# Kernel optimization log

Measured on AMD Instinct MI355X. Metric: run time of the kernel, lower is better.

The kernel has to match this reference:

```python
import jax, jax.numpy as jnp
import numpy as np

G = 32; N = G * G          # gridsize, num_nodes per graph
A = 16                      # n_agents
B = 32                      # batch_size
E = 4096                    # edges per graph (~4-neighbor grid)
F_IN = 16                   # input_dim
H = 64                      # hidden_dim
L = 3                       # n_graph_layers
MID = F_IN + L * H          # 208
CAT = 2 * MID + H           # 480
MIN_VAL = -1e8


def _layer_norm(x, g, b, eps=1e-5):
    m = x.mean(-1, keepdims=True)
    v = x.var(-1, keepdims=True)
    return (x - m) * jax.lax.rsqrt(v + eps) * g + b


def setup_inputs() -> dict:
    key = jax.random.key(0)
    ks = jax.random.split(key, 16)
    inp = {}
    inp["graph_nodes"] = jax.random.normal(ks[0], (B, N, F_IN), jnp.float32)
    inp["graph_edge_links"] = jax.random.randint(ks[1], (B, 2, E), 0, N)
    inp["agent_locations"] = jax.random.randint(ks[2], (B, A), 0, N)
    inp["mask"] = jax.random.bernoulli(ks[3], 0.5, (B, A * N))
    inp["dist_matrix"] = jax.random.uniform(ks[4], (N, N), jnp.float32)
    dims = [F_IN] + [H] * L
    k = 5
    for l in range(L):
        inp[f"conv{l}_W"] = jax.random.normal(ks[k], (dims[l], H), jnp.float32) * 0.05
        inp[f"conv{l}_b"] = jnp.zeros((H,), jnp.float32)
        inp[f"conv{l}_g"] = jnp.ones((H,), jnp.float32)
        inp[f"conv{l}_beta"] = jnp.zeros((H,), jnp.float32)
        k += 1
    inp["edges_W"] = jax.random.normal(ks[k], (1, H), jnp.float32) * 0.05
    inp["edges_b"] = jnp.zeros((H,), jnp.float32)
    inp["actor1_W"] = jax.random.normal(ks[k + 1], (CAT, MID), jnp.float32) * 0.05
    inp["actor1_b"] = jnp.zeros((MID,), jnp.float32)
    inp["bn_g"] = jnp.ones((MID,), jnp.float32)
    inp["bn_b"] = jnp.zeros((MID,), jnp.float32)
    inp["actor2_W"] = jax.random.normal(ks[k + 2], (MID, 1), jnp.float32) * 0.05
    inp["actor2_b"] = jnp.zeros((1,), jnp.float32)
    return inp


def reference(graph_nodes, graph_edge_links, agent_locations, mask, dist_matrix,
              conv0_W, conv0_b, conv0_g, conv0_beta,
              conv1_W, conv1_b, conv1_g, conv1_beta,
              conv2_W, conv2_b, conv2_g, conv2_beta,
              edges_W, edges_b, actor1_W, actor1_b, bn_g, bn_b,
              actor2_W, actor2_b):
    # --- batch graphs: offset node indices per graph (Batch.from_data_list) ---
    x = graph_nodes.reshape(B * N, F_IN)
    offs = (jnp.arange(B) * N)[:, None, None]
    ei = (graph_edge_links + offs).transpose(1, 0, 2).reshape(2, B * E)
    src, dst = ei[0], ei[1]

    conv_params = [(conv0_W, conv0_b, conv0_g, conv0_beta),
                   (conv1_W, conv1_b, conv1_g, conv1_beta),
                   (conv2_W, conv2_b, conv2_g, conv2_beta)]
    outs = [x]
    for W, bb, g, beta in conv_params:
        # GINConv with eps=-1: (1+eps)*x_i == 0, so out = mlp(sum_j x_j)
        agg = jax.ops.segment_sum(x[src], dst, num_segments=B * N)
        x = jax.nn.relu(_layer_norm(agg @ W + bb, g, beta))  # mlp relu; outer .relu() idempotent
        outs.append(x)
    xc = jnp.concatenate(outs, axis=1).reshape(B, N, MID)

    # --- all-pairs (agent, node) feature build ---
    a = jnp.take_along_axis(xc, agent_locations[:, :, None], axis=1)  # [B, A, MID]
    a = jnp.repeat(a, N, axis=1)                                      # [B, A*N, MID]
    bfeat = jnp.tile(xc, (1, A, 1))                                   # [B, A*N, MID]
    c = dist_matrix[agent_locations].reshape(B, A * N, 1)             # [B, A*N, 1]
    c = c @ edges_W + edges_b                                         # [B, A*N, H]
    h = jnp.concatenate([a, bfeat, c], axis=2).reshape(-1, CAT)

    h = h @ actor1_W + actor1_b
    mu = h.mean(0)
    var = h.var(0)
    h = (h - mu) * jax.lax.rsqrt(var + 1e-5) * bn_g + bn_b  # BatchNorm1d, training stats
    h = jax.nn.relu(h)
    logits = (h @ actor2_W + actor2_b).reshape(B, A * N)
    logits = jnp.where(mask, logits, MIN_VAL)
    return jax.nn.softmax(logits, axis=1)
```

## Files before the change

### kernel.cpp

```cpp
#include <hip/hip_runtime.h>
#include <cstddef>

#define B_    32
#define N_    1024
#define E_    4096
#define A_    16
#define FIN_  16
#define H_    64
#define MID_  208
#define NODES (B_ * N_)
#define NEDGE (B_ * E_)
#define ROWS  (B_ * A_ * N_)
#define AN_   (A_ * N_)

__device__ __forceinline__ float readlane_f(float v, int l) {
  return __uint_as_float(__builtin_amdgcn_readlane(__float_as_uint(v), l));
}

__global__ __launch_bounds__(256) void k_front(const int* __restrict__ el,
                                               const float* __restrict__ dist,
                                               const int* __restrict__ loc,
                                               const float* __restrict__ W1,
                                               const float* __restrict__ eW,
                                               const float* __restrict__ eb,
                                               const float* __restrict__ b1,
                                               int* __restrict__ rowptr,
                                               int* __restrict__ counts,
                                               int* __restrict__ ssrc,
                                               float* __restrict__ d1row,
                                               float* __restrict__ c2row,
                                               float* __restrict__ e1,
                                               float* __restrict__ cu,
                                               float* __restrict__ base) {
  __shared__ int cnt[1024];
  __shared__ int cur[1024];
  __shared__ int part[256];
  __shared__ int ssrcS[4096];
  __shared__ int loc_s[16];
  int blk = blockIdx.x, t = threadIdx.x;
  if (blk < 32) {
    int b = blk;
    for (int i = t; i < 1024; i += 256) cnt[i] = 0;
    __syncthreads();
    const int* srcp = el + b * (2 * E_);
    const int* dstp = srcp + E_;
    for (int i = t; i < E_; i += 256) atomicAdd(&cnt[dstp[i]], 1);
    __syncthreads();
    int4 c4 = *(const int4*)&cnt[t * 4];
    int s = c4.x + c4.y + c4.z + c4.w;
    part[t] = s;
    __syncthreads();
    for (int off = 1; off < 256; off <<= 1) {
      int v = (t >= off) ? part[t - off] : 0;
      __syncthreads();
      part[t] += v;
      __syncthreads();
    }
    int prev = (t == 0) ? 0 : part[t - 1];
    int p0 = prev, p1 = p0 + c4.x, p2 = p1 + c4.y, p3 = p2 + c4.z;
    *(int4*)&rowptr[b * 1024 + t * 4] = make_int4(p0 + b * E_, p1 + b * E_, p2 + b * E_, p3 + b * E_);
    *(int4*)&counts[b * 1024 + t * 4] = c4;
    cur[t * 4 + 0] = p0;
    cur[t * 4 + 1] = p1;
    cur[t * 4 + 2] = p2;
    cur[t * 4 + 3] = p3;
    __syncthreads();
    for (int i = t; i < E_; i += 256) {
      int dl = dstp[i];
      int sl = srcp[i];
      int pos = atomicAdd(&cur[dl], 1);
      ssrcS[pos] = b * N_ + sl;
    }
    __syncthreads();
    for (int i = t; i < E_; i += 256) ssrc[b * E_ + i] = ssrcS[i];
  } else if (blk < 288) {
    int lane = t & 63, w = t >> 6;
    int r = (blk - 32) * 4 + w;
    const float* dr = dist + (size_t)r * N_;
    float s = 0.f, c2 = 0.f;
#pragma unroll
    for (int k = 0; k < 16; k++) {
      float v = dr[lane + 64 * k];
      s += v;
      c2 = fmaf(v, v, c2);
    }
#pragma unroll
    for (int o = 32; o > 0; o >>= 1) { s += __shfl_xor(s, o); c2 += __shfl_xor(c2, o); }
    if (lane == 0) { d1row[r] = s; c2row[r] = c2; }
  } else if (blk < 320) {
    int b = blk - 288;
    if (t < 16) loc_s[t] = loc[b * 16 + t];
    __syncthreads();
    float e4[4] = {0.f, 0.f, 0.f, 0.f};
    for (int a = 0; a < 16; a++) {
      const float* dr = dist + (size_t)loc_s[a] * N_;
#pragma unroll
      for (int k = 0; k < 4; k++) e4[k] += dr[t + 256 * k];
    }
#pragma unroll
    for (int k = 0; k < 4; k++) e1[b * N_ + t + 256 * k] = e4[k];
  } else {
    int j = t;
    if (j < MID_) {
      float c = 0.f, bs = 0.f;
      for (int k = 0; k < H_; k++) {
        float w = W1[(2 * MID_ + k) * MID_ + j];
        c = fmaf(eW[k], w, c);
        bs = fmaf(eb[k], w, bs);
      }
      cu[j] = c;
      base[j] = bs + b1[j];
    }
  }
}

template <int FINT, bool COPYIN>
__global__ __launch_bounds__(256) void k_layer(const float* __restrict__ xin, int xstride, int in_off,
                                               float* __restrict__ xc, int out_off,
                                               const int* __restrict__ rowptr,
                                               const int* __restrict__ counts,
                                               const int* __restrict__ ssrc,
                                               const float* __restrict__ W,
                                               const float* __restrict__ bias,
                                               const float* __restrict__ g,
                                               const float* __restrict__ beta) {
  int t = threadIdx.x, lane = t & 63, w = t >> 6;
  float Wcol[FINT];
#pragma unroll
  for (int f = 0; f < FINT; f++) Wcol[f] = W[f * 64 + lane];
  float bv = bias[lane], gv = g[lane], bev = beta[lane];
  constexpr int CH = 64 / FINT;
  int f = lane & (FINT - 1);
  int ch = (FINT == 64) ? 0 : (lane >> 4);
  int blk = blockIdx.x;
  int xcd = blk & 7, kk = blk >> 3;
  int graph = xcd * 4 + (kk >> 5);
  int nblk = kk & 31;
  int nbase = graph * N_ + nblk * 32 + w * 8;

  float agg[8];
#pragma unroll
  for (int nn = 0; nn < 8; nn++) {
    int node = nbase + nn;
    int r0 = rowptr[node];
    int deg = counts[node];
    float a0 = 0.f, a1 = 0.f, a2 = 0.f, a3 = 0.f;
    int e = ch;
    for (; e + 3 * CH < deg; e += 4 * CH) {
      int s0 = ssrc[r0 + e];
      int s1 = ssrc[r0 + e + CH];
      int s2 = ssrc[r0 + e + 2 * CH];
      int s3 = ssrc[r0 + e + 3 * CH];
      a0 += xin[(size_t)s0 * xstride + in_off + f];
      a1 += xin[(size_t)s1 * xstride + in_off + f];
      a2 += xin[(size_t)s2 * xstride + in_off + f];
      a3 += xin[(size_t)s3 * xstride + in_off + f];
    }
    for (; e < deg; e += CH) {
      int s = ssrc[r0 + e];
      a0 += xin[(size_t)s * xstride + in_off + f];
    }
    agg[nn] = (a0 + a1) + (a2 + a3);
  }

#pragma unroll
  for (int nn = 0; nn < 8; nn++) {
    int node = nbase + nn;
    float aggf = agg[nn];
    float y0 = bv, y1 = 0.f, y2 = 0.f, y3 = 0.f;
#pragma unroll
    for (int l = 0; l < 64; l += 4) {
      y0 = fmaf(readlane_f(aggf, l + 0), Wcol[(l + 0) & (FINT - 1)], y0);
      y1 = fmaf(readlane_f(aggf, l + 1), Wcol[(l + 1) & (FINT - 1)], y1);
      y2 = fmaf(readlane_f(aggf, l + 2), Wcol[(l + 2) & (FINT - 1)], y2);
      y3 = fmaf(readlane_f(aggf, l + 3), Wcol[(l + 3) & (FINT - 1)], y3);
    }
    float y = (y0 + y1) + (y2 + y3);
    float m = y;
#pragma unroll
    for (int o = 32; o > 0; o >>= 1) m += __shfl_xor(m, o);
    m *= (1.f / 64.f);
    float d = y - m;
    float vv = d * d;
#pragma unroll
    for (int o = 32; o > 0; o >>= 1) vv += __shfl_xor(vv, o);
    vv *= (1.f / 64.f);
    float outv = fmaxf(d * rsqrtf(vv + 1e-5f) * gv + bev, 0.f);
    xc[(size_t)node * MID_ + out_off + lane] = outv;
    if (COPYIN) {
      if (lane < FIN_) xc[(size_t)node * MID_ + lane] = xin[(size_t)node * FIN_ + lane];
    }
  }
}

template <int NR>
__device__ __forceinline__ void gemm_sc(const float* __restrict__ xc,
                                        const float* __restrict__ W1,
                                        int row0w, int j0, float acc[NR][4]) {
  const float* Bbase = W1 + (size_t)MID_ * MID_;
  const float* Arow = xc + (size_t)row0w * MID_;
#pragma unroll
  for (int r = 0; r < NR; r++)
#pragma unroll
    for (int q = 0; q < 4; q++) acc[r][q] = 0.f;

#pragma unroll 2
  for (int c = 0; c < 52; c++) {
    int k = c * 4;
    float4 a[NR];
    const float* ap = Arow + k;
#pragma unroll
    for (int r = 0; r < NR; r++) a[r] = *(const float4*)(ap + r * MID_);
#pragma unroll
    for (int q = 0; q < 4; q++) {
      float4 bq = *(const float4*)(Bbase + (size_t)(k + q) * MID_ + j0);
#pragma unroll
      for (int r = 0; r < NR; r++) {
        float ar = (q == 0) ? a[r].x : (q == 1) ? a[r].y : (q == 2) ? a[r].z : a[r].w;
        acc[r][0] = fmaf(ar, bq.x, acc[r][0]);
        acc[r][1] = fmaf(ar, bq.y, acc[r][1]);
        acc[r][2] = fmaf(ar, bq.z, acc[r][2]);
        acc[r][3] = fmaf(ar, bq.w, acc[r][3]);
      }
    }
  }
}

#define TSTR 105
__global__ __launch_bounds__(128) void k_p1(const float* __restrict__ xc,
                                            const float* __restrict__ W1,
                                            const float* __restrict__ e1,
                                            const int* __restrict__ loc,
                                            float* __restrict__ SBp,
                                            float* __restrict__ pBT,
                                            float* __restrict__ pA) {
  __shared__ float smem[1680];
  int t = threadIdx.x, lane = t & 63;
  int w = __builtin_amdgcn_readfirstlane(t >> 6);
  int blk = blockIdx.x;
  if (blk < 2048) {
    int row0 = blk * 16;
    int row0w = row0 + w * 8;
    int j0 = lane * 4;
    float acc[8][4];
    gemm_sc<8>(xc, W1, row0w, j0, acc);
    const float* ep = e1 + row0w;
    float4 e0 = *(const float4*)(ep);
    float4 e4 = *(const float4*)(ep + 4);
    float ev[8] = {e0.x, e0.y, e0.z, e0.w, e4.x, e4.y, e4.z, e4.w};
    if (j0 < MID_) {
      float s1[4] = {0, 0, 0, 0}, s2[4] = {0, 0, 0, 0}, se[4] = {0, 0, 0, 0};
#pragma unroll
      for (int r = 0; r < 8; r++) {
#pragma unroll
        for (int q = 0; q < 4; q++) {
          float v = acc[r][q];
          s1[q] += v;
          s2[q] = fmaf(v, v, s2[q]);
          se[q] = fmaf(v, ev[r], se[q]);
        }
      }
#pragma unroll
      for (int q = 0; q < 4; q++) {
        smem[w * 624 + j0 + q] = s1[q];
        smem[w * 624 + 208 + j0 + q] = s2[q];
        smem[w * 624 + 416 + j0 + q] = se[q];
      }
    }
    __syncthreads();
    for (int idx = t; idx < 624; idx += 128) {
      SBp[(size_t)blk * 624 + idx] = smem[idx] + smem[624 + idx];
    }
#pragma unroll
    for (int half = 0; half < 2; half++) {
      int lo = half * 104;
      __syncthreads();
      if (j0 >= lo && j0 < lo + 104) {
        int jc = j0 - lo;
#pragma unroll
        for (int r = 0; r < 8; r++) {
          int ba = (w * 8 + r) * TSTR + jc;
          smem[ba + 0] = acc[r][0];
          smem[ba + 1] = acc[r][1];
          smem[ba + 2] = acc[r][2];
          smem[ba + 3] = acc[r][3];
        }
      }
      __syncthreads();
      int jb = lo + w * 52;
      int node = lane & 15;
      int jo = lane >> 4;
      for (int jj = 0; jj < 52; jj += 4) {
        int j = jb + jj + jo;
        pBT[(size_t)j * NODES + row0 + node] = smem[node * TSTR + (j - lo)];
      }
    }
  } else {
    int ab = blk - 2048;
    int b = ab >> 4;
    int node = b * N_ + loc[ab];
    float* xr = smem;
    for (int i = t; i < MID_; i += 128) xr[i] = xc[(size_t)node * MID_ + i];
    __syncthreads();
    for (int j = t; j < MID_; j += 128) {
      float acc = 0.f;
      for (int i = 0; i < MID_; i++) acc = fmaf(xr[i], W1[i * MID_ + j], acc);
      pA[ab * MID_ + j] = acc;
    }
  }
}

__global__ __launch_bounds__(256) void k_fin(const float* __restrict__ SBp,
                                             const float* __restrict__ pA,
                                             const float* __restrict__ cu,
                                             const float* __restrict__ base,
                                             const float* __restrict__ d1row,
                                             const float* __restrict__ c2row,
                                             const int* __restrict__ loc,
                                             const float* __restrict__ bng,
                                             const float* __restrict__ bnb,
                                             const float* __restrict__ W2,
                                             float* __restrict__ vaT,
                                             float* __restrict__ wpack4) {
  __shared__ float utmp[1536 + 192];
  __shared__ float redm[4];
  __shared__ float reds[4];
  __shared__ float bcast[2];
  int t = threadIdx.x, lane = t & 63, w = t >> 6;
  int j = blockIdx.x;
  float cuj = cu[j], bj = base[j];
  int bb = t >> 3, ii = t & 7;
  float q1 = 0, q2 = 0, q3 = 0, t1 = 0, t2 = 0, t3 = 0;
#pragma unroll
  for (int i = ii * 8; i < ii * 8 + 8; i++) {
    const float* sp = SBp + (size_t)(bb * 64 + i) * 624;
    q1 += sp[j];
    q2 += sp[208 + j];
    q3 += sp[416 + j];
  }
#pragma unroll
  for (int a = ii * 2; a < ii * 2 + 2; a++) {
    int r = bb * 16 + a;
    float pa = pA[r * MID_ + j] + bj;
    t1 += pa;
    t2 = fmaf(pa, pa, t2);
    t3 = fmaf(pa, d1row[loc[r]], t3);
  }
  utmp[0 * 256 + t] = q1;
  utmp[1 * 256 + t] = q2;
  utmp[2 * 256 + t] = q3;
  utmp[3 * 256 + t] = t1;
  utmp[4 * 256 + t] = t2;
  utmp[5 * 256 + t] = t3;
  float p1 = 0.f, p2 = 0.f;
#pragma unroll
  for (int r = t * 2; r < t * 2 + 2; r++) {
    int l = loc[r];
    p1 += d1row[l];
    p2 += c2row[l];
  }
#pragma unroll
  for (int o = 32; o > 0; o >>= 1) { p1 += __shfl_xor(p1, o); p2 += __shfl_xor(p2, o); }
  if (lane == 0) { redm[w] = p1; reds[w] = p2; }
  __syncthreads();
  if (t < 192) {
    int s = t >> 5, b32 = t & 31;
    float ssum = 0.f;
#pragma unroll
    for (int i = 0; i < 8; i++) ssum += utmp[s * 256 + b32 * 8 + i];
    utmp[1536 + s * 32 + b32] = ssum;
  }
  __syncthreads();
  if (t == 0) {
    float Sc1 = (redm[0] + redm[1]) + (redm[2] + redm[3]);
    float Sc2 = (reds[0] + reds[1]) + (reds[2] + reds[3]);
    double T1 = 0, T2 = 0, T3 = 0, cross = 0, sp1 = 0, sp2 = 0, spe = 0;
    for (int b = 0; b < 32; b++) {
      float sq1 = utmp[1536 + 0 * 32 + b];
      float sq2 = utmp[1536 + 1 * 32 + b];
      float sq3 = utmp[1536 + 2 * 32 + b];
      float pt1 = utmp[1536 + 3 * 32 + b];
      float pt2 = utmp[1536 + 4 * 32 + b];
      float pt3 = utmp[1536 + 5 * 32 + b];
      T1 += pt1; T2 += pt2; T3 += pt3;
      cross += (double)pt1 * sq1;
      sp1 += sq1; sp2 += sq2; spe += sq3;
    }
    double s1 = 1024.0 * T1 + 16.0 * sp1 + (double)cuj * Sc1;
    double s2 = 1024.0 * T2 + 16.0 * sp2 + (double)cuj * cuj * Sc2 +
                2.0 * (cross + (double)cuj * (T3 + spe));
    double mu = s1 * (1.0 / (double)ROWS);
    double var = s2 * (1.0 / (double)ROWS) - mu * mu;
    float sc = (float)(1.0 / sqrt(var + 1e-5)) * bng[j];
    float sh = bnb[j] - (float)mu * sc;
    bcast[0] = sc;
    bcast[1] = sh;
    wpack4[4 * j + 0] = sc;
    wpack4[4 * j + 1] = cuj * sc;
    wpack4[4 * j + 2] = W2[j];
    wpack4[4 * j + 3] = 0.f;
  }
  __syncthreads();
  float sc = bcast[0], sh = bcast[1];
#pragma unroll
  for (int r = t * 2; r < t * 2 + 2; r++) {
    int b = r >> 4, a = r & 15;
    float pa = pA[r * MID_ + j] + bj;
    vaT[((size_t)b * MID_ + j) * 16 + a] = pa * sc + sh;
  }
}

__global__ __launch_bounds__(256) void k_logits(const float* __restrict__ pBT,
                                                const float* __restrict__ vaT,
                                                const float* __restrict__ wpack4,
                                                const float* __restrict__ dist,
                                                const int* __restrict__ loc,
                                                const int* __restrict__ mask,
                                                const float* __restrict__ b2,
                                                float* __restrict__ lg,
                                                float2* __restrict__ Psm) {
  __shared__ float vaS[MID_ * 16];
  __shared__ float accL[4][8][64];
  __shared__ int loc_s[16];
  __shared__ float redm[4];
  __shared__ float reds[4];
  int t = threadIdx.x, lane = t & 63;
  int w = __builtin_amdgcn_readfirstlane(t >> 6);
  int b = blockIdx.y, nt = blockIdx.x;
  int n0 = nt * 64;
  if (t < 16) loc_s[t] = loc[b * 16 + t];
  for (int i = t; i < MID_ * 16; i += 256) vaS[i] = vaT[(size_t)b * MID_ * 16 + i];
  __syncthreads();
  float c[16];
#pragma unroll
  for (int a = 0; a < 16; a++) c[a] = dist[(size_t)loc_s[a] * N_ + n0 + lane];
  float acc16[16];
#pragma unroll
  for (int a = 0; a < 16; a++) acc16[a] = 0.f;
  const float4* wp = (const float4*)wpack4;
  int ng = b * N_ + n0 + lane;
  int jb = w * 52;
#pragma unroll 4
  for (int jj = 0; jj < 52; jj++) {
    int j = jb + jj;
    float pbv = pBT[(size_t)j * NODES + ng];
    float4 wv = wp[j];
    float pbs = pbv * wv.x;
    const float* va = &vaS[j * 16];
#pragma unroll
    for (int a = 0; a < 16; a++) {
      float h = fmaf(c[a], wv.y, va[a] + pbs);
      h = fmaxf(h, 0.f);
      acc16[a] = fmaf(h, wv.z, acc16[a]);
    }
  }

  float b2v = b2[0];
  float sv[4];
  int ois[4];
  unsigned mk = 0;
#pragma unroll
  for (int half = 0; half < 2; half++) {
#pragma unroll
    for (int a8 = 0; a8 < 8; a8++) accL[t >> 6][a8][lane] = acc16[half * 8 + a8];
    __syncthreads();
#pragma unroll
    for (int p = 0; p < 2; p++) {
      int idx = p * 256 + t;
      int a8 = idx >> 6, nn = idx & 63;
      float s = (accL[0][a8][nn] + accL[1][a8][nn]) +
                (accL[2][a8][nn] + accL[3][a8][nn]) + b2v;
      int a = half * 8 + a8;
      int oi = b * AN_ + a * N_ + n0 + nn;
      int iv = half * 2 + p;
      bool m_ = mask[oi] != 0;
      sv[iv] = m_ ? s : -1e8f;
      ois[iv] = oi;
      mk |= (m_ ? 1u : 0u) << iv;
    }
    __syncthreads();
  }

  float mx = fmaxf(fmaxf(sv[0], sv[1]), fmaxf(sv[2], sv[3]));
#pragma unroll
  for (int o = 32; o > 0; o >>= 1) mx = fmaxf(mx, __shfl_xor(mx, o));
  if (lane == 0) redm[t >> 6] = mx;
  __syncthreads();
  mx = fmaxf(fmaxf(redm[0], redm[1]), fmaxf(redm[2], redm[3]));
  float ssum = 0.f;
#pragma unroll
  for (int iv = 0; iv < 4; iv++) {
    float pv = ((mk >> iv) & 1u) ? expf(sv[iv] - mx) : 0.f;
    lg[ois[iv]] = pv;
    ssum += pv;
  }
#pragma unroll
  for (int o = 32; o > 0; o >>= 1) ssum += __shfl_xor(ssum, o);
  if (lane == 0) reds[t >> 6] = ssum;
  __syncthreads();
  if (t == 0) Psm[b * 16 + nt] = make_float2(mx, (reds[0] + reds[1]) + (reds[2] + reds[3]));
}

__global__ __launch_bounds__(256) void k_sm2(const float* __restrict__ lg,
                                             const float2* __restrict__ P,
                                             float* __restrict__ out) {
  __shared__ float scs[16];
  int b = blockIdx.y, x = blockIdx.x, t = threadIdx.x;
  float M = -3.0e38f;
  float2 pr[16];
#pragma unroll
  for (int k = 0; k < 16; k++) {
    pr[k] = P[b * 16 + k];
    M = fmaxf(M, pr[k].x);
  }
  float S = 0.f;
#pragma unroll
  for (int k = 0; k < 16; k++) S += pr[k].y * expf(pr[k].x - M);
  float inv = 1.0f / S;
  if (t < 16) scs[t] = expf(pr[t].x - M) * inv;
  __syncthreads();
  const float* lb = lg + b * AN_ + x * 2048;
  float* ob = out + b * AN_ + x * 2048;
#pragma unroll
  for (int k = 0; k < 8; k++) {
    int i = t + 256 * k;
    int n = (x * 2048 + i) & 1023;
    ob[i] = lb[i] * scs[n >> 6];
  }
}

extern "C" void kernel_launch(void* const* d_in, const int* in_sizes, int n_in,
                              void* d_out, int out_size, void* d_ws, size_t ws_size,
                              hipStream_t stream) {
  const float* gn = (const float*)d_in[0];
  const int* el = (const int*)d_in[1];
  const int* loc = (const int*)d_in[2];
  const int* mask = (const int*)d_in[3];
  const float* dist = (const float*)d_in[4];
  const float* c0W = (const float*)d_in[5];
  const float* c0b = (const float*)d_in[6];
  const float* c0g = (const float*)d_in[7];
  const float* c0be = (const float*)d_in[8];
  const float* c1W = (const float*)d_in[9];
  const float* c1b = (const float*)d_in[10];
  const float* c1g = (const float*)d_in[11];
  const float* c1be = (const float*)d_in[12];
  const float* c2W = (const float*)d_in[13];
  const float* c2b = (const float*)d_in[14];
  const float* c2g = (const float*)d_in[15];
  const float* c2be = (const float*)d_in[16];
  const float* eW = (const float*)d_in[17];
  const float* eb = (const float*)d_in[18];
  const float* W1 = (const float*)d_in[19];
  const float* b1 = (const float*)d_in[20];
  const float* bng = (const float*)d_in[21];
  const float* bnb = (const float*)d_in[22];
  const float* W2 = (const float*)d_in[23];
  const float* b2 = (const float*)d_in[24];
  float* out = (float*)d_out;

  char* p = (char*)d_ws;
  auto alloc = [&](size_t bytes) {
    char* r = p;
    p += (bytes + 255) & ~(size_t)255;
    return r;
  };
  int* counts = (int*)alloc((size_t)NODES * 4);
  int* rowptr = (int*)alloc((size_t)NODES * 4);
  int* ssrc = (int*)alloc((size_t)NEDGE * 4);
  float* xc = (float*)alloc((size_t)NODES * MID_ * 4);
  float* pBT = (float*)alloc((size_t)NODES * MID_ * 4);
  float* pA = (float*)alloc((size_t)512 * MID_ * 4);
  float* cu = (float*)alloc(256 * 4);
  float* base = (float*)alloc(256 * 4);
  float* d1row = (float*)alloc((size_t)N_ * 4);
  float* c2row = (float*)alloc((size_t)N_ * 4);
  float* e1 = (float*)alloc((size_t)B_ * N_ * 4);
  float* SBp = (float*)alloc((size_t)2048 * 624 * 4);
  float* vaT = (float*)alloc((size_t)B_ * MID_ * 16 * 4);
  float* wpack4 = (float*)alloc((size_t)MID_ * 4 * 4);
  float* lg = (float*)alloc((size_t)ROWS * 4);
  float2* Psm = (float2*)alloc((size_t)B_ * 16 * 8);

  k_front<<<321, 256, 0, stream>>>(el, dist, loc, W1, eW, eb, b1,
                                   rowptr, counts, ssrc, d1row, c2row, e1, cu, base);

  k_layer<16, true><<<1024, 256, 0, stream>>>(gn, FIN_, 0, xc, 16, rowptr, counts, ssrc, c0W, c0b, c0g, c0be);
  k_layer<64, false><<<1024, 256, 0, stream>>>(xc, MID_, 16, xc, 80, rowptr, counts, ssrc, c1W, c1b, c1g, c1be);
  k_layer<64, false><<<1024, 256, 0, stream>>>(xc, MID_, 80, xc, 144, rowptr, counts, ssrc, c2W, c2b, c2g, c2be);

  k_p1<<<2560, 128, 0, stream>>>(xc, W1, e1, loc, SBp, pBT, pA);
  k_fin<<<208, 256, 0, stream>>>(SBp, pA, cu, base, d1row, c2row, loc, bng, bnb, W2, vaT, wpack4);

  k_logits<<<dim3(16, 32), 256, 0, stream>>>(pBT, vaT, wpack4, dist, loc, mask, b2, lg, Psm);
  k_sm2<<<dim3(8, 32), 256, 0, stream>>>(lg, Psm, out);
}
```

Measured before the change: 268.4 us.

## Compute node projection GEMM with split-bf16 MFMA and move column stats to k_fin

Replaces the scalar FP32 xc·W1B GEMM in k_p1 with MFMA 16x16x32 bf16 instructions. Both operands are split into hi and lo bf16 parts and three products are summed to approximate FP32 accuracy. A pre-transposed, padded bf16 copy of W1B is built in extra k_front blocks. The per-block column statistics (sum, sum of squares, dot with e1) are no longer produced in k_p1 through SBp; k_fin now recomputes them by streaming pBT and e1. This trades the FP32 FMA cost for matrix-core throughput, at the price of a small precision loss and an extra full read of pBT in k_fin.

New measurement: 259.8 us. 1.03x faster.

```diff
diff --git a/kernel.cpp b/kernel.cpp
--- a/kernel.cpp
+++ b/kernel.cpp
@@ -15,6 +15,25 @@
 
 __device__ __forceinline__ float readlane_f(float v, int l) {
   return __uint_as_float(__builtin_amdgcn_readlane(__float_as_uint(v), l));
+}
+
+typedef __attribute__((ext_vector_type(8))) __bf16 bf16x8;
+typedef __attribute__((ext_vector_type(4))) float f32x4;
+
+__device__ __forceinline__ f32x4 mfma16(bf16x8 a, bf16x8 b, f32x4 c) {
+  return __builtin_amdgcn_mfma_f32_16x16x32_bf16(a, b, c, 0, 0, 0);
+}
+
+__device__ __forceinline__ void cvt8(const float* __restrict__ p, bf16x8& hi, bf16x8& lo) {
+  float4 v0 = *(const float4*)p;
+  float4 v1 = *(const float4*)(p + 4);
+  float vv[8] = {v0.x, v0.y, v0.z, v0.w, v1.x, v1.y, v1.z, v1.w};
+#pragma unroll
+  for (int i = 0; i < 8; i++) {
+    __bf16 h = (__bf16)vv[i];
+    hi[i] = h;
+    lo[i] = (__bf16)(vv[i] - (float)h);
+  }
 }
 
 __global__ __launch_bounds__(256) void k_front(const int* __restrict__ el,
@@ -31,7 +50,9 @@
                                                float* __restrict__ c2row,
                                                float* __restrict__ e1,
                                                float* __restrict__ cu,
-                                               float* __restrict__ base) {
+                                               float* __restrict__ base,
+                                               __bf16* __restrict__ W1BTh,
+                                               __bf16* __restrict__ W1BTl) {
   __shared__ int cnt[1024];
   __shared__ int cur[1024];
   __shared__ int part[256];
@@ -99,7 +120,7 @@
     }
 #pragma unroll
     for (int k = 0; k < 4; k++) e1[b * N_ + t + 256 * k] = e4[k];
-  } else {
+  } else if (blk == 320) {
     int j = t;
     if (j < MID_) {
       float c = 0.f, bs = 0.f;
@@ -110,6 +131,14 @@
       }
       cu[j] = c;
       base[j] = bs + b1[j];
+    }
+  } else {
+    int jr = blk - 321;
+    if (t < 224) {
+      float v = (t < MID_) ? W1[(size_t)(MID_ + t) * MID_ + jr] : 0.f;
+      __bf16 h = (__bf16)v;
+      W1BTh[jr * 224 + t] = h;
+      W1BTl[jr * 224 + t] = (__bf16)(v - (float)h);
     }
   }
 }
@@ -193,124 +222,85 @@
   }
 }
 
-template <int NR>
-__device__ __forceinline__ void gemm_sc(const float* __restrict__ xc,
-                                        const float* __restrict__ W1,
-                                        int row0w, int j0, float acc[NR][4]) {
-  const float* Bbase = W1 + (size_t)MID_ * MID_;
-  const float* Arow = xc + (size_t)row0w * MID_;
-#pragma unroll
-  for (int r = 0; r < NR; r++)
-#pragma unroll
-    for (int q = 0; q < 4; q++) acc[r][q] = 0.f;
-
-#pragma unroll 2
-  for (int c = 0; c < 52; c++) {
-    int k = c * 4;
-    float4 a[NR];
-    const float* ap = Arow + k;
-#pragma unroll
-    for (int r = 0; r < NR; r++) a[r] = *(const float4*)(ap + r * MID_);
-#pragma unroll
-    for (int q = 0; q < 4; q++) {
-      float4 bq = *(const float4*)(Bbase + (size_t)(k + q) * MID_ + j0);
-#pragma unroll
-      for (int r = 0; r < NR; r++) {
-        float ar = (q == 0) ? a[r].x : (q == 1) ? a[r].y : (q == 2) ? a[r].z : a[r].w;
-        acc[r][0] = fmaf(ar, bq.x, acc[r][0]);
-        acc[r][1] = fmaf(ar, bq.y, acc[r][1]);
-        acc[r][2] = fmaf(ar, bq.z, acc[r][2]);
-        acc[r][3] = fmaf(ar, bq.w, acc[r][3]);
-      }
-    }
-  }
-}
-
-#define TSTR 105
-__global__ __launch_bounds__(128) void k_p1(const float* __restrict__ xc,
+__global__ __launch_bounds__(256) void k_p1(const float* __restrict__ xc,
                                             const float* __restrict__ W1,
-                                            const float* __restrict__ e1,
+                                            const __bf16* __restrict__ W1BTh,
+                                            const __bf16* __restrict__ W1BTl,
                                             const int* __restrict__ loc,
-                                            float* __restrict__ SBp,
                                             float* __restrict__ pBT,
                                             float* __restrict__ pA) {
-  __shared__ float smem[1680];
+  __shared__ float xr[MID_];
   int t = threadIdx.x, lane = t & 63;
-  int w = __builtin_amdgcn_readfirstlane(t >> 6);
+  int w = t >> 6;
   int blk = blockIdx.x;
-  if (blk < 2048) {
-    int row0 = blk * 16;
-    int row0w = row0 + w * 8;
-    int j0 = lane * 4;
-    float acc[8][4];
-    gemm_sc<8>(xc, W1, row0w, j0, acc);
-    const float* ep = e1 + row0w;
-    float4 e0 = *(const float4*)(ep);
-    float4 e4 = *(const float4*)(ep + 4);
-    float ev[8] = {e0.x, e0.y, e0.z, e0.w, e4.x, e4.y, e4.z, e4.w};
-    if (j0 < MID_) {
-      float s1[4] = {0, 0, 0, 0}, s2[4] = {0, 0, 0, 0}, se[4] = {0, 0, 0, 0};
-#pragma unroll
-      for (int r = 0; r < 8; r++) {
-#pragma unroll
-        for (int q = 0; q < 4; q++) {
-          float v = acc[r][q];
-          s1[q] += v;
-          s2[q] = fmaf(v, v, s2[q]);
-          se[q] = fmaf(v, ev[r], se[q]);
+  if (blk < 1024) {
+    int nb = blk * 32;
+    int q = lane >> 4, li = lane & 15;
+    int jt0 = (w == 0) ? 0 : (w == 1) ? 4 : (w == 2) ? 7 : 10;
+    int njt = (w == 0) ? 4 : 3;
+    f32x4 zero4 = {0.f, 0.f, 0.f, 0.f};
+    f32x4 acc0[4], acc1[4];
+#pragma unroll
+    for (int i = 0; i < 4; i++) { acc0[i] = zero4; acc1[i] = zero4; }
+    const float* xr0 = xc + (size_t)(nb + li) * MID_;
+    const float* xr1 = xc + (size_t)(nb + 16 + li) * MID_;
+    for (int kc = 0; kc < 7; kc++) {
+      int k0 = kc * 32 + q * 8;
+      bf16x8 b0h, b0l, b1h, b1l;
+      if (k0 < MID_) {
+        cvt8(xr0 + k0, b0h, b0l);
+        cvt8(xr1 + k0, b1h, b1l);
+      } else {
+#pragma unroll
+        for (int i = 0; i < 8; i++) {
+          b0h[i] = (__bf16)0.f; b0l[i] = (__bf16)0.f;
+          b1h[i] = (__bf16)0.f; b1l[i] = (__bf16)0.f;
         }
       }
 #pragma unroll
-      for (int q = 0; q < 4; q++) {
-        smem[w * 624 + j0 + q] = s1[q];
-        smem[w * 624 + 208 + j0 + q] = s2[q];
-        smem[w * 624 + 416 + j0 + q] = se[q];
-      }
-    }
-    __syncthreads();
-    for (int idx = t; idx < 624; idx += 128) {
-      SBp[(size_t)blk * 624 + idx] = smem[idx] + smem[624 + idx];
-    }
-#pragma unroll
-    for (int half = 0; half < 2; half++) {
-      int lo = half * 104;
-      __syncthreads();
-      if (j0 >= lo && j0 < lo + 104) {
-        int jc = j0 - lo;
-#pragma unroll
-        for (int r = 0; r < 8; r++) {
-          int ba = (w * 8 + r) * TSTR + jc;
-          smem[ba + 0] = acc[r][0];
-          smem[ba + 1] = acc[r][1];
-          smem[ba + 2] = acc[r][2];
-          smem[ba + 3] = acc[r][3];
+      for (int jj = 0; jj < 4; jj++) {
+        if (jj < njt) {
+          int jt = jt0 + jj;
+          bf16x8 ah = *(const bf16x8*)(W1BTh + (size_t)(jt * 16 + li) * 224 + k0);
+          bf16x8 al = *(const bf16x8*)(W1BTl + (size_t)(jt * 16 + li) * 224 + k0);
+          acc0[jj] = mfma16(ah, b0h, acc0[jj]);
+          acc0[jj] = mfma16(ah, b0l, acc0[jj]);
+          acc0[jj] = mfma16(al, b0h, acc0[jj]);
+          acc1[jj] = mfma16(ah, b1h, acc1[jj]);
+          acc1[jj] = mfma16(ah, b1l, acc1[jj]);
+          acc1[jj] = mfma16(al, b1h, acc1[jj]);
         }
       }
-      __syncthreads();
-      int jb = lo + w * 52;
-      int node = lane & 15;
-      int jo = lane >> 4;
-      for (int jj = 0; jj < 52; jj += 4) {
-        int j = jb + jj + jo;
-        pBT[(size_t)j * NODES + row0 + node] = smem[node * TSTR + (j - lo)];
+    }
+#pragma unroll
+    for (int jj = 0; jj < 4; jj++) {
+      if (jj < njt) {
+        int jt = jt0 + jj;
+#pragma unroll
+        for (int r = 0; r < 4; r++) {
+          int j = jt * 16 + q * 4 + r;
+          float* pb = pBT + (size_t)j * NODES + nb + li;
+          pb[0] = acc0[jj][r];
+          pb[16] = acc1[jj][r];
+        }
       }
     }
   } else {
-    int ab = blk - 2048;
+    int ab = blk - 1024;
     int b = ab >> 4;
     int node = b * N_ + loc[ab];
-    float* xr = smem;
-    for (int i = t; i < MID_; i += 128) xr[i] = xc[(size_t)node * MID_ + i];
-    __syncthreads();
-    for (int j = t; j < MID_; j += 128) {
+    for (int i = t; i < MID_; i += 256) xr[i] = xc[(size_t)node * MID_ + i];
+    __syncthreads();
+    if (t < MID_) {
       float acc = 0.f;
-      for (int i = 0; i < MID_; i++) acc = fmaf(xr[i], W1[i * MID_ + j], acc);
-      pA[ab * MID_ + j] = acc;
-    }
-  }
-}
-
-__global__ __launch_bounds__(256) void k_fin(const float* __restrict__ SBp,
+      for (int i = 0; i < MID_; i++) acc = fmaf(xr[i], W1[i * MID_ + t], acc);
+      pA[ab * MID_ + t] = acc;
+    }
+  }
+}
+
+__global__ __launch_bounds__(256) void k_fin(const float* __restrict__ pBT,
+                                             const float* __restrict__ e1,
                                              const float* __restrict__ pA,
                                              const float* __restrict__ cu,
                                              const float* __restrict__ base,
@@ -329,18 +319,19 @@
   int t = threadIdx.x, lane = t & 63, w = t >> 6;
   int j = blockIdx.x;
   float cuj = cu[j], bj = base[j];
-  int bb = t >> 3, ii = t & 7;
-  float q1 = 0, q2 = 0, q3 = 0, t1 = 0, t2 = 0, t3 = 0;
-#pragma unroll
-  for (int i = ii * 8; i < ii * 8 + 8; i++) {
-    const float* sp = SBp + (size_t)(bb * 64 + i) * 624;
-    q1 += sp[j];
-    q2 += sp[208 + j];
-    q3 += sp[416 + j];
-  }
-#pragma unroll
-  for (int a = ii * 2; a < ii * 2 + 2; a++) {
-    int r = bb * 16 + a;
+  const float* pr = pBT + (size_t)j * NODES + t * 128;
+  const float* er = e1 + t * 128;
+  float q1 = 0.f, q2 = 0.f, q3 = 0.f;
+  for (int i = 0; i < 128; i += 4) {
+    float4 v = *(const float4*)(pr + i);
+    float4 e = *(const float4*)(er + i);
+    q1 += (v.x + v.y) + (v.z + v.w);
+    q2 = fmaf(v.x, v.x, fmaf(v.y, v.y, fmaf(v.z, v.z, fmaf(v.w, v.w, q2))));
+    q3 = fmaf(v.x, e.x, fmaf(v.y, e.y, fmaf(v.z, e.z, fmaf(v.w, e.w, q3))));
+  }
+  float t1 = 0.f, t2 = 0.f, t3 = 0.f;
+#pragma unroll
+  for (int r = t * 2; r < t * 2 + 2; r++) {
     float pa = pA[r * MID_ + j] + bj;
     t1 += pa;
     t2 = fmaf(pa, pa, t2);
@@ -576,21 +567,23 @@
   float* d1row = (float*)alloc((size_t)N_ * 4);
   float* c2row = (float*)alloc((size_t)N_ * 4);
   float* e1 = (float*)alloc((size_t)B_ * N_ * 4);
-  float* SBp = (float*)alloc((size_t)2048 * 624 * 4);
   float* vaT = (float*)alloc((size_t)B_ * MID_ * 16 * 4);
   float* wpack4 = (float*)alloc((size_t)MID_ * 4 * 4);
   float* lg = (float*)alloc((size_t)ROWS * 4);
   float2* Psm = (float2*)alloc((size_t)B_ * 16 * 8);
-
-  k_front<<<321, 256, 0, stream>>>(el, dist, loc, W1, eW, eb, b1,
-                                   rowptr, counts, ssrc, d1row, c2row, e1, cu, base);
+  __bf16* W1BTh = (__bf16*)alloc((size_t)MID_ * 224 * 2);
+  __bf16* W1BTl = (__bf16*)alloc((size_t)MID_ * 224 * 2);
+
+  k_front<<<529, 256, 0, stream>>>(el, dist, loc, W1, eW, eb, b1,
+                                   rowptr, counts, ssrc, d1row, c2row, e1, cu, base,
+                                   W1BTh, W1BTl);
 
   k_layer<16, true><<<1024, 256, 0, stream>>>(gn, FIN_, 0, xc, 16, rowptr, counts, ssrc, c0W, c0b, c0g, c0be);
   k_layer<64, false><<<1024, 256, 0, stream>>>(xc, MID_, 16, xc, 80, rowptr, counts, ssrc, c1W, c1b, c1g, c1be);
   k_layer<64, false><<<1024, 256, 0, stream>>>(xc, MID_, 80, xc, 144, rowptr, counts, ssrc, c2W, c2b, c2g, c2be);
 
-  k_p1<<<2560, 128, 0, stream>>>(xc, W1, e1, loc, SBp, pBT, pA);
-  k_fin<<<208, 256, 0, stream>>>(SBp, pA, cu, base, d1row, c2row, loc, bng, bnb, W2, vaT, wpack4);
+  k_p1<<<1536, 256, 0, stream>>>(xc, W1, W1BTh, W1BTl, loc, pBT, pA);
+  k_fin<<<208, 256, 0, stream>>>(pBT, e1, pA, cu, base, d1row, c2row, loc, bng, bnb, W2, vaT, wpack4);
 
   k_logits<<<dim3(16, 32), 256, 0, stream>>>(pBT, vaT, wpack4, dist, loc, mask, b2, lg, Psm);
   k_sm2<<<dim3(8, 32), 256, 0, stream>>>(lg, Psm, out);
```
